# Kernel optimization log

Measured on AMD Instinct MI355X. Metric: run time of the kernel, lower is better.

The kernel has to match this reference:

```python
import jax, jax.numpy as jnp
import numpy as np

B, S, CIN, H, W = 4, 16, 32, 64, 64
HID = 64


def conv2d(x, w, b=None):
    # x: (N,C,H,W), w: (O,I,kh,kw), stride 1, padding 1 (SAME for k=3)
    y = jax.lax.conv_general_dilated(
        x, w, window_strides=(1, 1), padding=[(1, 1), (1, 1)],
        dimension_numbers=("NCHW", "OIHW", "NCHW"))
    if b is not None:
        y = y + b[None, :, None, None]
    return y


def log_g(x):
    # log of g(x) = x+0.5 if x>=0 else sigmoid(x); safe double-where for grads
    pos = jnp.where(x >= 0, x, 0.0)
    return jnp.where(x >= 0, jnp.log(pos + 0.5), -jax.nn.softplus(-x))


def mingru_gate_hidden(gate, hidden, h_prev):
    # gate, hidden: (B,S,C,H,W); h_prev: (B,1,C,H,W), positive
    log_z = -jax.nn.softplus(-gate)        # log sigmoid(gate)
    log_coeffs = -jax.nn.softplus(gate)    # log (1 - sigmoid(gate))
    log_h0 = jnp.log(h_prev)
    log_values = jnp.concatenate([log_h0, log_z + log_g(hidden)], axis=1)  # (B,S+1,...)
    a_star = jnp.pad(jnp.cumsum(log_coeffs, axis=1),
                     ((0, 0), (1, 0), (0, 0), (0, 0), (0, 0)))             # (B,S+1,...)
    log_h = a_star + jax.lax.cumlogsumexp(log_values - a_star, axis=1)
    return jnp.exp(log_h)[:, 1:]  # (B,S,C,H,W)


def _layer(inp, Wg, bg, Rw):
    b_, s_ = inp.shape[:2]
    flat = inp.reshape(b_ * s_, *inp.shape[2:])
    y = conv2d(flat, Wg, bg)
    y = y.reshape(b_, s_, y.shape[1], y.shape[2], y.shape[3])
    gate, hidden = jnp.split(y, 2, axis=2)
    # init_hidden_state: g(zeros) == 0.5 everywhere
    h0 = jnp.full((b_, 1) + gate.shape[2:], 0.5, dtype=inp.dtype)
    out = mingru_gate_hidden(gate, hidden, h0)
    h_next = out[:, -1:]
    if Rw is not None:
        res = conv2d(flat, Rw).reshape(b_, s_, -1, out.shape[3], out.shape[4])
    else:
        res = inp  # res_align is Identity
    return out + res, h_next


def setup_inputs() -> dict:
    key = jax.random.key(0)
    ks = jax.random.split(key, 4)
    x = jax.random.normal(ks[0], (B, S, CIN, H, W), jnp.float32)
    s0 = 1.0 / np.sqrt(CIN * 9)
    s1 = 1.0 / np.sqrt(HID * 9)
    W0 = jax.random.normal(ks[1], (2 * HID, CIN, 3, 3), jnp.float32) * s0
    b0 = jnp.zeros((2 * HID,), jnp.float32)
    R0 = jax.random.normal(ks[2], (HID, CIN, 3, 3), jnp.float32) * s0  # res align 32->64
    W1 = jax.random.normal(ks[3], (2 * HID, HID, 3, 3), jnp.float32) * s1
    b1 = jnp.zeros((2 * HID,), jnp.float32)
    return {"x": x, "W0": W0, "b0": b0, "R0": R0, "W1": W1, "b1": b1}


def reference(x, W0, b0, R0, W1, b1):
    out, h0 = _layer(x, W0, b0, R0)
    out, h1 = _layer(out, W1, b1, None)
    return out, h0, h1
```

## Files before the change

### kernel.cpp

```cpp
#include <hip/hip_runtime.h>

typedef short short8  __attribute__((ext_vector_type(8)));
typedef short shortx4 __attribute__((ext_vector_type(4)));
typedef float floatx4 __attribute__((ext_vector_type(4)));
typedef unsigned short u16;

static __device__ __forceinline__ float bits2f(u16 s) {
    return __builtin_bit_cast(float, (unsigned)s << 16);
}
static __device__ __forceinline__ u16 f2bits(float f) {
    return __builtin_bit_cast(u16, (__bf16)f);
}

#define SS 16

__global__ void prep_transpose_kernel(const float* __restrict__ x, u16* __restrict__ xT,
                                      const float* W0, const float* R0, const float* W1,
                                      u16* wt0f, u16* wt1) {
    const int bid = blockIdx.x;
    if (bid < 4096) {
        const int img = bid >> 6, h = bid & 63;
        const int gq = threadIdx.x & 3, w = threadIdx.x >> 2;
        short8 o;
#pragma unroll
        for (int k = 0; k < 8; ++k)
            o[k] = (short)f2bits(x[((size_t)img * 32 + gq * 8 + k) * 4096 + h * 64 + w]);
        ((short8*)xT)[((size_t)(img * 64 + h) * 64 + w) * 4 + gq] = o;
        return;
    }
    const int i = (bid - 4096) * 256 + threadIdx.x;
    if (i < 55296) {
        const int t = i / 6144, r = i % 6144, ko = r >> 5, ci = r & 31;
        wt0f[i] = f2bits(ko < 128 ? W0[(ko * 32 + ci) * 9 + t]
                                  : R0[((ko - 128) * 32 + ci) * 9 + t]);
    } else if (i < 55296 + 73728) {
        const int j = i - 55296;
        const int t = j / 8192, r = j % 8192, ko = r >> 6, ci = r & 63;
        wt1[j] = f2bits(W1[(ko * 64 + ci) * 9 + t]);
    }
}

__global__ __launch_bounds__(256, 2)
void fused_layer0_kernel(const u16* __restrict__ X, const u16* __restrict__ wt,
                         const float* __restrict__ bias,
                         u16* __restrict__ x1out, float* __restrict__ hlast) {
    __shared__ short8 lds[2][4 * 18 * 4];

    const int tid = threadIdx.x;
    const int l   = tid & 63;
    const int wv  = tid >> 6;
    const int c16 = l & 15;
    const int q16 = l >> 4;

    const int bid = blockIdx.x;
    const int b   = bid >> 7;
    const int h0  = ((bid >> 2) & 31) * 2;
    const int w0  = (bid & 3) * 16;

    const short8* wtv = (const short8*)wt;
    short8 af[9][3];
#pragma unroll
    for (int t = 0; t < 9; ++t)
#pragma unroll
        for (int g = 0; g < 3; ++g)
            af[t][g] = wtv[(size_t)(t * 192 + (wv + g * 4) * 16 + c16) * 4 + q16];

    const floatx4 biasg = *(const floatx4*)(bias + wv * 16 + q16 * 4);
    const floatx4 biash = *(const floatx4*)(bias + 64 + wv * 16 + q16 * 4);

    int ldsoff[2], goff[2];
    bool gval[2];
#pragma unroll
    for (int k = 0; k < 2; ++k) {
        const int idx = tid + k * 256;
        const int row = (idx >= 216) ? 3 : (idx >= 144) ? 2 : (idx >= 72) ? 1 : 0;
        const int rem = idx - row * 72;
        const int colrel = rem >> 2, q = rem & 3;
        const int hh = h0 - 1 + row;
        const int gc = w0 - 1 + colrel;
        ldsoff[k] = (row * 18 + colrel) * 4 + ((q + colrel) & 3);
        gval[k]   = (idx < 288) && ((unsigned)hh < 64u) && ((unsigned)gc < 64u);
        goff[k]   = (hh * 64 + gc) * 4 + q;
    }
    const bool k1 = (tid < 32);

    float hs[2][4];
#pragma unroll
    for (int m = 0; m < 2; ++m)
#pragma unroll
        for (int r = 0; r < 4; ++r) hs[m][r] = 0.5f;

    const short8* Xg = (const short8*)X;
    const short8 z8 = {0, 0, 0, 0, 0, 0, 0, 0};
    shortx4* x1v = (shortx4*)x1out;

    short8 vW0, vW1;
    {
        const short8* base = Xg + (size_t)(b * 16) * 16384;
        vW0 = gval[0] ? base[goff[0]] : z8;
        vW1 = gval[1] ? base[goff[1]] : z8;
    }
    lds[0][ldsoff[0]] = vW0;
    if (k1) lds[0][ldsoff[1]] = vW1;
    {
        const short8* base = Xg + (size_t)(b * 16 + 1) * 16384;
        vW0 = gval[0] ? base[goff[0]] : z8;
        vW1 = gval[1] ? base[goff[1]] : z8;
    }
    __syncthreads();

#pragma unroll
    for (int s = 0; s < SS; ++s) {
        const int cur = s & 1;

        if (s + 1 < SS) {
            lds[cur ^ 1][ldsoff[0]] = vW0;
            if (k1) lds[cur ^ 1][ldsoff[1]] = vW1;
        }
        if (s + 2 < SS) {
            const short8* base = Xg + (size_t)(b * 16 + s + 2) * 16384;
            vW0 = gval[0] ? base[goff[0]] : z8;
            vW1 = gval[1] ? base[goff[1]] : z8;
        }

        floatx4 acc[3][2];
#pragma unroll
        for (int m = 0; m < 2; ++m) {
            acc[0][m] = biasg; acc[1][m] = biash;
            acc[2][m] = floatx4{0.0f, 0.0f, 0.0f, 0.0f};
        }
#pragma unroll
        for (int t = 0; t < 9; ++t) {
            const int dy = t / 3, dx = t - dy * 3;
#pragma unroll
            for (int m = 0; m < 2; ++m) {
                const int row = m + dy;
                const int lc  = c16 + dx;
                const short8 bf = lds[cur][(row * 18 + lc) * 4 + ((q16 + lc) & 3)];
#pragma unroll
                for (int g = 0; g < 3; ++g)
                    acc[g][m] = __builtin_amdgcn_mfma_f32_16x16x32_bf16(
                        af[t][g], bf, acc[g][m], 0, 0, 0);
            }
        }

#pragma unroll
        for (int m = 0; m < 2; ++m) {
            shortx4 ov;
#pragma unroll
            for (int r = 0; r < 4; ++r) {
                const float g   = acc[0][m][r];
                const float hid = acc[1][m][r];
                const float zz  = 1.0f / (1.0f + __expf(-g));
                const float gg  = (hid >= 0.0f) ? (hid + 0.5f)
                                                : (1.0f / (1.0f + __expf(-hid)));
                hs[m][r] = hs[m][r] + zz * (gg - hs[m][r]);
                ov[r] = (short)f2bits(hs[m][r] + acc[2][m][r]);
            }
            const size_t px = ((size_t)(b * 16 + s) * 64 + (h0 + m)) * 64
                              + w0 + c16;
            x1v[px * 16 + wv * 4 + q16] = ov;
        }
        __syncthreads();
    }

    float* hp = hlast + ((size_t)(b * 64) + (wv * 16 + q16 * 4)) * 4096
                      + h0 * 64 + w0 + c16;
#pragma unroll
    for (int m = 0; m < 2; ++m)
#pragma unroll
        for (int r = 0; r < 4; ++r)
            hp[(size_t)r * 4096 + m * 64] = hs[m][r];
}

__global__ __launch_bounds__(256, 2)
void fused_layer1_kernel(const u16* __restrict__ X, const u16* __restrict__ wt,
                         const float* __restrict__ bias,
                         float* __restrict__ out, float* __restrict__ hlast) {
    __shared__ short8 lds[2][4 * 18 * 8];

    const int tid = threadIdx.x;
    const int l   = tid & 63;
    const int wv  = tid >> 6;
    const int c16 = l & 15;
    const int q16 = l >> 4;

    const int bid = blockIdx.x;
    const int b   = bid >> 7;
    const int h0  = ((bid >> 2) & 31) * 2;
    const int w0  = (bid & 3) * 16;

    const short8* wtv = (const short8*)wt;
    short8 af[2][9][2];
#pragma unroll
    for (int ch = 0; ch < 2; ++ch)
#pragma unroll
        for (int t = 0; t < 9; ++t)
#pragma unroll
            for (int g = 0; g < 2; ++g)
                af[ch][t][g] =
                    wtv[(size_t)(t * 128 + (wv + g * 4) * 16 + c16) * 8 + ch * 4 + q16];

    const floatx4 biasg = *(const floatx4*)(bias + wv * 16 + q16 * 4);
    const floatx4 biash = *(const floatx4*)(bias + 64 + wv * 16 + q16 * 4);

    int ldsoff[3], goff[3];
    bool gval[3];
#pragma unroll
    for (int k = 0; k < 3; ++k) {
        const int idx = tid + k * 256;
        const int row = (idx >= 432) ? 3 : (idx >= 288) ? 2 : (idx >= 144) ? 1 : 0;
        const int rem = idx - row * 144;
        const int colrel = rem >> 3, q = rem & 7;
        const int hh = h0 - 1 + row;
        const int gc = w0 - 1 + colrel;
        ldsoff[k] = (row * 18 + colrel) * 8 + ((q + colrel) & 7);
        gval[k]   = (idx < 576) && ((unsigned)hh < 64u) && ((unsigned)gc < 64u);
        goff[k]   = (hh * 64 + gc) * 8 + q;
    }
    const bool k2 = (tid < 64);

    float hs[2][4];
#pragma unroll
    for (int m = 0; m < 2; ++m)
#pragma unroll
        for (int r = 0; r < 4; ++r) hs[m][r] = 0.5f;

    float* op = out + ((size_t)(b * 16) * 64 + (wv * 16 + q16 * 4)) * 4096
                    + h0 * 64 + w0 + c16;

    const short8* Xg = (const short8*)X;
    const short8 z8 = {0, 0, 0, 0, 0, 0, 0, 0};

    short8 vW0, vW1, vW2;
    {
        const short8* base = Xg + (size_t)(b * 16) * 32768;
        vW0 = gval[0] ? base[goff[0]] : z8;
        vW1 = gval[1] ? base[goff[1]] : z8;
        vW2 = gval[2] ? base[goff[2]] : z8;
    }
    lds[0][ldsoff[0]] = vW0;
    lds[0][ldsoff[1]] = vW1;
    if (k2) lds[0][ldsoff[2]] = vW2;
    {
        const short8* base = Xg + (size_t)(b * 16 + 1) * 32768;
        vW0 = gval[0] ? base[goff[0]] : z8;
        vW1 = gval[1] ? base[goff[1]] : z8;
        vW2 = gval[2] ? base[goff[2]] : z8;
    }
    __syncthreads();

#pragma unroll
    for (int s = 0; s < SS; ++s) {
        const int cur = s & 1;

        if (s + 1 < SS) {
            lds[cur ^ 1][ldsoff[0]] = vW0;
            lds[cur ^ 1][ldsoff[1]] = vW1;
            if (k2) lds[cur ^ 1][ldsoff[2]] = vW2;
        }
        if (s + 2 < SS) {
            const short8* base = Xg + (size_t)(b * 16 + s + 2) * 32768;
            vW0 = gval[0] ? base[goff[0]] : z8;
            vW1 = gval[1] ? base[goff[1]] : z8;
            vW2 = gval[2] ? base[goff[2]] : z8;
        }

        floatx4 acc[2][2];
#pragma unroll
        for (int m = 0; m < 2; ++m) { acc[0][m] = biasg; acc[1][m] = biash; }
#pragma unroll
        for (int ch = 0; ch < 2; ++ch)
#pragma unroll
            for (int t = 0; t < 9; ++t) {
                const int dy = t / 3, dx = t - dy * 3;
#pragma unroll
                for (int m = 0; m < 2; ++m) {
                    const int row = m + dy;
                    const int lc  = c16 + dx;
                    const short8 bf =
                        lds[cur][(row * 18 + lc) * 8 + ((ch * 4 + q16 + lc) & 7)];
                    acc[0][m] = __builtin_amdgcn_mfma_f32_16x16x32_bf16(
                        af[ch][t][0], bf, acc[0][m], 0, 0, 0);
                    acc[1][m] = __builtin_amdgcn_mfma_f32_16x16x32_bf16(
                        af[ch][t][1], bf, acc[1][m], 0, 0, 0);
                }
            }

        float* ops = op + (size_t)s * 262144;
        const int qres = wv * 2 + (q16 >> 1);
#pragma unroll
        for (int m = 0; m < 2; ++m) {
            const int rowc = 1 + m;
            const int lcc  = 1 + c16;
            const shortx4 rr = *(const shortx4*)(
                (const short*)&lds[cur][(rowc * 18 + lcc) * 8 + ((qres + lcc) & 7)]
                + (q16 & 1) * 4);
#pragma unroll
            for (int r = 0; r < 4; ++r) {
                const float g   = acc[0][m][r];
                const float hid = acc[1][m][r];
                const float zz  = 1.0f / (1.0f + __expf(-g));
                const float gg  = (hid >= 0.0f) ? (hid + 0.5f)
                                                : (1.0f / (1.0f + __expf(-hid)));
                hs[m][r] = hs[m][r] + zz * (gg - hs[m][r]);
                const float o = hs[m][r] + bits2f((u16)rr[r]);
                ops[(size_t)r * 4096 + m * 64] = o;
            }
        }
        __syncthreads();
    }

    float* hp = hlast + ((size_t)(b * 64) + (wv * 16 + q16 * 4)) * 4096
                      + h0 * 64 + w0 + c16;
#pragma unroll
    for (int m = 0; m < 2; ++m)
#pragma unroll
        for (int r = 0; r < 4; ++r)
            hp[(size_t)r * 4096 + m * 64] = hs[m][r];
}

extern "C" void kernel_launch(void* const* d_in, const int* in_sizes, int n_in,
                              void* d_out, int out_size, void* d_ws, size_t ws_size,
                              hipStream_t stream) {
    const float* x  = (const float*)d_in[0];
    const float* W0 = (const float*)d_in[1];
    const float* b0 = (const float*)d_in[2];
    const float* R0 = (const float*)d_in[3];
    const float* W1 = (const float*)d_in[4];
    const float* b1 = (const float*)d_in[5];

    float* out = (float*)d_out;
    float* h0o = out + (size_t)16777216;
    float* h1o = h0o + (size_t)1048576;

    char* ws = (char*)d_ws;
    u16*   wt0f = (u16*)ws;
    u16*   wt1  = (u16*)(ws + 110592);
    u16*   xT   = (u16*)(ws + (size_t)(1  << 20));
    u16*   x1   = (u16*)(ws + (size_t)(18 << 20));

    prep_transpose_kernel<<<4600, 256, 0, stream>>>(x, xT, W0, R0, W1, wt0f, wt1);

    fused_layer0_kernel<<<512, 256, 0, stream>>>(xT, wt0f, b0, x1, h0o);

    fused_layer1_kernel<<<512, 256, 0, stream>>>(x1, wt1, b1, out, h1o);
}
```

Before: 191.3 us.

## Halve rows per block, single-buffer LDS, and double the grid for occupancy

Each block of both fused layer kernels now handles one output row instead of two, and the launch grid doubles to 1024 blocks. The LDS tile shrinks to a single 3-row halo buffer with a sync before compute, replacing the double buffer and two-step prefetch, and launch bounds rise to allow more resident blocks. The goal is more parallelism and occupancy on a 256-CU device that previously had only 512 blocks. The cost is less reuse of the halo and weight registers per block, an extra barrier per timestep, and a shallower load pipeline.

```diff
diff --git a/kernel.cpp b/kernel.cpp
--- a/kernel.cpp
+++ b/kernel.cpp
@@ -40,11 +40,11 @@
     }
 }
 
-__global__ __launch_bounds__(256, 2)
+__global__ __launch_bounds__(256, 3)
 void fused_layer0_kernel(const u16* __restrict__ X, const u16* __restrict__ wt,
                          const float* __restrict__ bias,
                          u16* __restrict__ x1out, float* __restrict__ hlast) {
-    __shared__ short8 lds[2][4 * 18 * 4];
+    __shared__ short8 lds[3 * 18 * 4];
 
     const int tid = threadIdx.x;
     const int l   = tid & 63;
@@ -53,8 +53,8 @@
     const int q16 = l >> 4;
 
     const int bid = blockIdx.x;
-    const int b   = bid >> 7;
-    const int h0  = ((bid >> 2) & 31) * 2;
+    const int b   = bid >> 8;
+    const int h0  = (bid >> 2) & 63;
     const int w0  = (bid & 3) * 16;
 
     const short8* wtv = (const short8*)wt;
@@ -68,97 +68,71 @@
     const floatx4 biasg = *(const floatx4*)(bias + wv * 16 + q16 * 4);
     const floatx4 biash = *(const floatx4*)(bias + 64 + wv * 16 + q16 * 4);
 
-    int ldsoff[2], goff[2];
-    bool gval[2];
-#pragma unroll
-    for (int k = 0; k < 2; ++k) {
-        const int idx = tid + k * 256;
-        const int row = (idx >= 216) ? 3 : (idx >= 144) ? 2 : (idx >= 72) ? 1 : 0;
+    const bool k0 = (tid < 216);
+    int ldsoff0 = 0, goff0 = 0;
+    bool gval0 = false;
+    {
+        const int idx = tid;
+        const int row = (idx >= 144) ? 2 : (idx >= 72) ? 1 : 0;
         const int rem = idx - row * 72;
         const int colrel = rem >> 2, q = rem & 3;
         const int hh = h0 - 1 + row;
         const int gc = w0 - 1 + colrel;
-        ldsoff[k] = (row * 18 + colrel) * 4 + ((q + colrel) & 3);
-        gval[k]   = (idx < 288) && ((unsigned)hh < 64u) && ((unsigned)gc < 64u);
-        goff[k]   = (hh * 64 + gc) * 4 + q;
-    }
-    const bool k1 = (tid < 32);
-
-    float hs[2][4];
-#pragma unroll
-    for (int m = 0; m < 2; ++m)
-#pragma unroll
-        for (int r = 0; r < 4; ++r) hs[m][r] = 0.5f;
+        ldsoff0 = (row * 18 + colrel) * 4 + ((q + colrel) & 3);
+        gval0   = k0 && ((unsigned)hh < 64u) && ((unsigned)gc < 64u);
+        goff0   = (hh * 64 + gc) * 4 + q;
+    }
+
+    float hs[4];
+#pragma unroll
+    for (int r = 0; r < 4; ++r) hs[r] = 0.5f;
 
     const short8* Xg = (const short8*)X;
     const short8 z8 = {0, 0, 0, 0, 0, 0, 0, 0};
     shortx4* x1v = (shortx4*)x1out;
 
-    short8 vW0, vW1;
+    short8 vW0;
     {
         const short8* base = Xg + (size_t)(b * 16) * 16384;
-        vW0 = gval[0] ? base[goff[0]] : z8;
-        vW1 = gval[1] ? base[goff[1]] : z8;
-    }
-    lds[0][ldsoff[0]] = vW0;
-    if (k1) lds[0][ldsoff[1]] = vW1;
-    {
-        const short8* base = Xg + (size_t)(b * 16 + 1) * 16384;
-        vW0 = gval[0] ? base[goff[0]] : z8;
-        vW1 = gval[1] ? base[goff[1]] : z8;
-    }
-    __syncthreads();
-
-#pragma unroll
+        vW0 = gval0 ? base[goff0] : z8;
+    }
+
     for (int s = 0; s < SS; ++s) {
-        const int cur = s & 1;
+        if (k0) lds[ldsoff0] = vW0;
+        __syncthreads();
 
         if (s + 1 < SS) {
-            lds[cur ^ 1][ldsoff[0]] = vW0;
-            if (k1) lds[cur ^ 1][ldsoff[1]] = vW1;
-        }
-        if (s + 2 < SS) {
-            const short8* base = Xg + (size_t)(b * 16 + s + 2) * 16384;
-            vW0 = gval[0] ? base[goff[0]] : z8;
-            vW1 = gval[1] ? base[goff[1]] : z8;
-        }
-
-        floatx4 acc[3][2];
-#pragma unroll
-        for (int m = 0; m < 2; ++m) {
-            acc[0][m] = biasg; acc[1][m] = biash;
-            acc[2][m] = floatx4{0.0f, 0.0f, 0.0f, 0.0f};
-        }
+            const short8* base = Xg + (size_t)(b * 16 + s + 1) * 16384;
+            vW0 = gval0 ? base[goff0] : z8;
+        }
+
+        floatx4 acc[3];
+        acc[0] = biasg; acc[1] = biash;
+        acc[2] = floatx4{0.0f, 0.0f, 0.0f, 0.0f};
 #pragma unroll
         for (int t = 0; t < 9; ++t) {
             const int dy = t / 3, dx = t - dy * 3;
-#pragma unroll
-            for (int m = 0; m < 2; ++m) {
-                const int row = m + dy;
-                const int lc  = c16 + dx;
-                const short8 bf = lds[cur][(row * 18 + lc) * 4 + ((q16 + lc) & 3)];
-#pragma unroll
-                for (int g = 0; g < 3; ++g)
-                    acc[g][m] = __builtin_amdgcn_mfma_f32_16x16x32_bf16(
-                        af[t][g], bf, acc[g][m], 0, 0, 0);
-            }
-        }
-
-#pragma unroll
-        for (int m = 0; m < 2; ++m) {
+            const int lc = c16 + dx;
+            const short8 bf = lds[(dy * 18 + lc) * 4 + ((q16 + lc) & 3)];
+#pragma unroll
+            for (int g = 0; g < 3; ++g)
+                acc[g] = __builtin_amdgcn_mfma_f32_16x16x32_bf16(
+                    af[t][g], bf, acc[g], 0, 0, 0);
+        }
+
+        {
             shortx4 ov;
 #pragma unroll
             for (int r = 0; r < 4; ++r) {
-                const float g   = acc[0][m][r];
-                const float hid = acc[1][m][r];
+                const float g   = acc[0][r];
+                const float hid = acc[1][r];
                 const float zz  = 1.0f / (1.0f + __expf(-g));
                 const float gg  = (hid >= 0.0f) ? (hid + 0.5f)
                                                 : (1.0f / (1.0f + __expf(-hid)));
-                hs[m][r] = hs[m][r] + zz * (gg - hs[m][r]);
-                ov[r] = (short)f2bits(hs[m][r] + acc[2][m][r]);
+                hs[r] = hs[r] + zz * (gg - hs[r]);
+                ov[r] = (short)f2bits(hs[r] + acc[2][r]);
             }
-            const size_t px = ((size_t)(b * 16 + s) * 64 + (h0 + m)) * 64
-                              + w0 + c16;
+            const size_t px = ((size_t)(b * 16 + s) * 64 + h0) * 64 + w0 + c16;
             x1v[px * 16 + wv * 4 + q16] = ov;
         }
         __syncthreads();
@@ -167,17 +141,15 @@
     float* hp = hlast + ((size_t)(b * 64) + (wv * 16 + q16 * 4)) * 4096
                       + h0 * 64 + w0 + c16;
 #pragma unroll
-    for (int m = 0; m < 2; ++m)
-#pragma unroll
-        for (int r = 0; r < 4; ++r)
-            hp[(size_t)r * 4096 + m * 64] = hs[m][r];
-}
-
-__global__ __launch_bounds__(256, 2)
+    for (int r = 0; r < 4; ++r)
+        hp[(size_t)r * 4096] = hs[r];
+}
+
+__global__ __launch_bounds__(256, 4)
 void fused_layer1_kernel(const u16* __restrict__ X, const u16* __restrict__ wt,
                          const float* __restrict__ bias,
                          float* __restrict__ out, float* __restrict__ hlast) {
-    __shared__ short8 lds[2][4 * 18 * 8];
+    __shared__ short8 lds[3 * 18 * 8];
 
     const int tid = threadIdx.x;
     const int l   = tid & 63;
@@ -186,8 +158,8 @@
     const int q16 = l >> 4;
 
     const int bid = blockIdx.x;
-    const int b   = bid >> 7;
-    const int h0  = ((bid >> 2) & 31) * 2;
+    const int b   = bid >> 8;
+    const int h0  = (bid >> 2) & 63;
     const int w0  = (bid & 3) * 16;
 
     const short8* wtv = (const short8*)wt;
@@ -204,27 +176,25 @@
     const floatx4 biasg = *(const floatx4*)(bias + wv * 16 + q16 * 4);
     const floatx4 biash = *(const floatx4*)(bias + 64 + wv * 16 + q16 * 4);
 
-    int ldsoff[3], goff[3];
-    bool gval[3];
-#pragma unroll
-    for (int k = 0; k < 3; ++k) {
+    int ldsoff[2], goff[2];
+    bool gval[2];
+#pragma unroll
+    for (int k = 0; k < 2; ++k) {
         const int idx = tid + k * 256;
-        const int row = (idx >= 432) ? 3 : (idx >= 288) ? 2 : (idx >= 144) ? 1 : 0;
+        const int row = (idx >= 288) ? 2 : (idx >= 144) ? 1 : 0;
         const int rem = idx - row * 144;
         const int colrel = rem >> 3, q = rem & 7;
         const int hh = h0 - 1 + row;
         const int gc = w0 - 1 + colrel;
         ldsoff[k] = (row * 18 + colrel) * 8 + ((q + colrel) & 7);
-        gval[k]   = (idx < 576) && ((unsigned)hh < 64u) && ((unsigned)gc < 64u);
+        gval[k]   = (idx < 432) && ((unsigned)hh < 64u) && ((unsigned)gc < 64u);
         goff[k]   = (hh * 64 + gc) * 8 + q;
     }
-    const bool k2 = (tid < 64);
-
-    float hs[2][4];
-#pragma unroll
-    for (int m = 0; m < 2; ++m)
-#pragma unroll
-        for (int r = 0; r < 4; ++r) hs[m][r] = 0.5f;
+    const bool k1 = (tid < 176);
+
+    float hs[4];
+#pragma unroll
+    for (int r = 0; r < 4; ++r) hs[r] = 0.5f;
 
     float* op = out + ((size_t)(b * 16) * 64 + (wv * 16 + q16 * 4)) * 4096
                     + h0 * 64 + w0 + c16;
@@ -232,80 +202,57 @@
     const short8* Xg = (const short8*)X;
     const short8 z8 = {0, 0, 0, 0, 0, 0, 0, 0};
 
-    short8 vW0, vW1, vW2;
+    short8 vW0, vW1;
     {
         const short8* base = Xg + (size_t)(b * 16) * 32768;
         vW0 = gval[0] ? base[goff[0]] : z8;
         vW1 = gval[1] ? base[goff[1]] : z8;
-        vW2 = gval[2] ? base[goff[2]] : z8;
-    }
-    lds[0][ldsoff[0]] = vW0;
-    lds[0][ldsoff[1]] = vW1;
-    if (k2) lds[0][ldsoff[2]] = vW2;
-    {
-        const short8* base = Xg + (size_t)(b * 16 + 1) * 32768;
-        vW0 = gval[0] ? base[goff[0]] : z8;
-        vW1 = gval[1] ? base[goff[1]] : z8;
-        vW2 = gval[2] ? base[goff[2]] : z8;
-    }
-    __syncthreads();
-
-#pragma unroll
+    }
+
     for (int s = 0; s < SS; ++s) {
-        const int cur = s & 1;
+        lds[ldsoff[0]] = vW0;
+        if (k1) lds[ldsoff[1]] = vW1;
+        __syncthreads();
 
         if (s + 1 < SS) {
-            lds[cur ^ 1][ldsoff[0]] = vW0;
-            lds[cur ^ 1][ldsoff[1]] = vW1;
-            if (k2) lds[cur ^ 1][ldsoff[2]] = vW2;
-        }
-        if (s + 2 < SS) {
-            const short8* base = Xg + (size_t)(b * 16 + s + 2) * 32768;
+            const short8* base = Xg + (size_t)(b * 16 + s + 1) * 32768;
             vW0 = gval[0] ? base[goff[0]] : z8;
             vW1 = gval[1] ? base[goff[1]] : z8;
-            vW2 = gval[2] ? base[goff[2]] : z8;
-        }
-
-        floatx4 acc[2][2];
-#pragma unroll
-        for (int m = 0; m < 2; ++m) { acc[0][m] = biasg; acc[1][m] = biash; }
+        }
+
+        floatx4 acc[2];
+        acc[0] = biasg; acc[1] = biash;
 #pragma unroll
         for (int ch = 0; ch < 2; ++ch)
 #pragma unroll
             for (int t = 0; t < 9; ++t) {
                 const int dy = t / 3, dx = t - dy * 3;
-#pragma unroll
-                for (int m = 0; m < 2; ++m) {
-                    const int row = m + dy;
-                    const int lc  = c16 + dx;
-                    const short8 bf =
-                        lds[cur][(row * 18 + lc) * 8 + ((ch * 4 + q16 + lc) & 7)];
-                    acc[0][m] = __builtin_amdgcn_mfma_f32_16x16x32_bf16(
-                        af[ch][t][0], bf, acc[0][m], 0, 0, 0);
-                    acc[1][m] = __builtin_amdgcn_mfma_f32_16x16x32_bf16(
-                        af[ch][t][1], bf, acc[1][m], 0, 0, 0);
-                }
+                const int lc = c16 + dx;
+                const short8 bf =
+                    lds[(dy * 18 + lc) * 8 + ((ch * 4 + q16 + lc) & 7)];
+                acc[0] = __builtin_amdgcn_mfma_f32_16x16x32_bf16(
+                    af[ch][t][0], bf, acc[0], 0, 0, 0);
+                acc[1] = __builtin_amdgcn_mfma_f32_16x16x32_bf16(
+                    af[ch][t][1], bf, acc[1], 0, 0, 0);
             }
 
         float* ops = op + (size_t)s * 262144;
         const int qres = wv * 2 + (q16 >> 1);
-#pragma unroll
-        for (int m = 0; m < 2; ++m) {
-            const int rowc = 1 + m;
-            const int lcc  = 1 + c16;
+        {
+            const int lcc = 1 + c16;
             const shortx4 rr = *(const shortx4*)(
-                (const short*)&lds[cur][(rowc * 18 + lcc) * 8 + ((qres + lcc) & 7)]
+                (const short*)&lds[(18 + lcc) * 8 + ((qres + lcc) & 7)]
                 + (q16 & 1) * 4);
 #pragma unroll
             for (int r = 0; r < 4; ++r) {
-                const float g   = acc[0][m][r];
-                const float hid = acc[1][m][r];
+                const float g   = acc[0][r];
+                const float hid = acc[1][r];
                 const float zz  = 1.0f / (1.0f + __expf(-g));
                 const float gg  = (hid >= 0.0f) ? (hid + 0.5f)
                                                 : (1.0f / (1.0f + __expf(-hid)));
-                hs[m][r] = hs[m][r] + zz * (gg - hs[m][r]);
-                const float o = hs[m][r] + bits2f((u16)rr[r]);
-                ops[(size_t)r * 4096 + m * 64] = o;
+                hs[r] = hs[r] + zz * (gg - hs[r]);
+                const float o = hs[r] + bits2f((u16)rr[r]);
+                ops[(size_t)r * 4096] = o;
             }
         }
         __syncthreads();
@@ -314,10 +261,8 @@
     float* hp = hlast + ((size_t)(b * 64) + (wv * 16 + q16 * 4)) * 4096
                       + h0 * 64 + w0 + c16;
 #pragma unroll
-    for (int m = 0; m < 2; ++m)
-#pragma unroll
-        for (int r = 0; r < 4; ++r)
-            hp[(size_t)r * 4096 + m * 64] = hs[m][r];
+    for (int r = 0; r < 4; ++r)
+        hp[(size_t)r * 4096] = hs[r];
 }
 
 extern "C" void kernel_launch(void* const* d_in, const int* in_sizes, int n_in,
@@ -342,7 +287,7 @@
 
     prep_transpose_kernel<<<4600, 256, 0, stream>>>(x, xT, W0, R0, W1, wt0f, wt1);
 
-    fused_layer0_kernel<<<512, 256, 0, stream>>>(xT, wt0f, b0, x1, h0o);
-
-    fused_layer1_kernel<<<512, 256, 0, stream>>>(x1, wt1, b1, out, h1o);
-}
+    fused_layer0_kernel<<<1024, 256, 0, stream>>>(xT, wt0f, b0, x1, h0o);
+
+    fused_layer1_kernel<<<1024, 256, 0, stream>>>(x1, wt1, b1, out, h1o);
+}
```

Measured after the change: 343.1 us. 1.79x slower.
